# Performance work log

Measured on AMD Instinct MI355X. Metric: run time of the kernel, lower is better.

## Reference

```python
import jax, jax.numpy as jnp
import numpy as np

NODE_SIZE = 500000
LINK_SIZE = 500
DIM = 128
NORM_P = 1
MARGIN = 1.0
BATCH = 16384


def setup_inputs() -> dict:
    key = jax.random.key(0)
    k1, k2, k3, k4, k5, k6, k7, k8 = jax.random.split(key, 8)
    ur_e = 6.0 / np.sqrt(DIM)
    ur_m = 6.0 / DIM
    node_w = jax.random.uniform(k1, (NODE_SIZE, DIM), jnp.float32, -ur_e, ur_e)
    link_w = jax.random.uniform(k2, (LINK_SIZE, DIM), jnp.float32, -ur_e, ur_e)
    transfer_w = jax.random.uniform(k3, (LINK_SIZE, DIM * DIM), jnp.float32, -ur_m, ur_m)
    sp = jax.random.randint(k4, (BATCH,), 0, NODE_SIZE)
    tp = jax.random.randint(k5, (BATCH,), 0, NODE_SIZE)
    sn = jax.random.randint(k6, (BATCH,), 0, NODE_SIZE)
    tn = jax.random.randint(k7, (BATCH,), 0, NODE_SIZE)
    r = jax.random.randint(k8, (BATCH,), 0, LINK_SIZE)
    return {"node_w": node_w, "link_w": link_w, "transfer_w": transfer_w,
            "sp": sp, "tp": tp, "sn": sn, "tn": tn, "r": r}


def _distance(node_w, link_w, transfer_w, s, r, t):
    # gather embeddings
    s_emb = node_w[s]                      # [B, D]
    t_emb = node_w[t]                      # [B, D]
    r_emb = link_w[r]                      # [B, D]
    M = transfer_w[r].reshape(-1, DIM, DIM)  # [B, D, D]
    # per-sample (1xD)x(DxD) matvec: e @ M
    s_proj = jnp.einsum('bd,bde->be', s_emb, M)
    t_proj = jnp.einsum('bd,bde->be', t_emb, M)
    diff = s_proj + r_emb - t_proj
    if NORM_P == 1:
        return jnp.sum(jnp.abs(diff), axis=1)
    return jnp.sum(jnp.abs(diff) ** NORM_P, axis=1) ** (1.0 / NORM_P)


def reference(node_w, link_w, transfer_w, sp, tp, sn, tn, r):
    pos = _distance(node_w, link_w, transfer_w, sp, r, tp)
    neg = _distance(node_w, link_w, transfer_w, sn, r, tn)
    # MarginRankingLoss with target = -1: max(0, (pos - neg) + margin)
    loss = jnp.maximum(pos - neg + MARGIN, 0.0)
    return jnp.mean(loss)
```

## Files before the change

kernel.cpp:

```cpp
#include <hip/hip_runtime.h>

#define BATCH 16384
#define DIM 128
#define NLINK 500
#define NG 16
#define CAP 128

__device__ __forceinline__ void gload_lds16(const float* g, float* l) {
    __builtin_amdgcn_global_load_lds(
        (const __attribute__((address_space(1))) void*)g,
        (__attribute__((address_space(3))) void*)l, 16, 0, 0);
}

__global__ void k_init(float* __restrict__ out) {
    if (threadIdx.x == 0) out[0] = 0.0f;
}

#define FMA4(acc, m, s)                                          \
    acc.x = fmaf(m.x, s, acc.x); acc.y = fmaf(m.y, s, acc.y);    \
    acc.z = fmaf(m.z, s, acc.z); acc.w = fmaf(m.w, s, acc.w);

#define STEP(M_, C_)                                             \
    FMA4(a0, M_, v0.C_) FMA4(a1, M_, v1.C_)                      \
    FMA4(a2, M_, v2.C_) FMA4(a3, M_, v3.C_)                      \
    FMA4(a4, M_, v4.C_) FMA4(a5, M_, v5.C_)                      \
    FMA4(a6, M_, v6.C_) FMA4(a7, M_, v7.C_)

__global__ __launch_bounds__(512, 2) void k_fused(
    const float* __restrict__ node_w, const float* __restrict__ link_w,
    const float* __restrict__ transfer_w,
    const int* __restrict__ sp, const int* __restrict__ tp,
    const int* __restrict__ sn, const int* __restrict__ tn,
    const int* __restrict__ r, float* __restrict__ out)
{
    __shared__ float Ms[DIM * DIM];
    __shared__ float dv[NG * 8 * DIM];
    __shared__ int   slist[CAP];
    __shared__ int   cnt;
    __shared__ float lossbuf[NG];

    const int link = blockIdx.x;
    const int t = threadIdx.x;
    const int g = t >> 5;
    const int q = t & 31;

    if (t == 0) cnt = 0;
    __syncthreads();

    int4 rv[8];
    #pragma unroll
    for (int j = 0; j < 8; j++) rv[j] = ((const int4*)r)[j * 512 + t];

    {
        const float* src = transfer_w + (size_t)link * (DIM * DIM);
        #pragma unroll
        for (int i = 0; i < 8; i++) {
            const int c = (t + 512 * i) * 4;
            gload_lds16(src + c, Ms + c);
        }
    }

    #pragma unroll
    for (int j = 0; j < 8; j++) {
        const int bi = (j * 512 + t) * 4;
        if (rv[j].x == link) slist[atomicAdd(&cnt, 1)] = bi;
        if (rv[j].y == link) slist[atomicAdd(&cnt, 1)] = bi + 1;
        if (rv[j].z == link) slist[atomicAdd(&cnt, 1)] = bi + 2;
        if (rv[j].w == link) slist[atomicAdd(&cnt, 1)] = bi + 3;
    }
    __syncthreads();

    const int count = cnt;
    float* gbase = dv + (g * 8) * DIM;
    const float4* M4 = (const float4*)Ms;
    float lsum = 0.0f;

    for (int u0 = 4 * g; u0 < count; u0 += 4 * NG) {
        const float4 re = ((const float4*)(link_w + (size_t)link * DIM))[q];

        const int b0 = slist[u0];
        const int b1 = slist[(u0 + 1 < count) ? u0 + 1 : count - 1];
        const int b2 = slist[(u0 + 2 < count) ? u0 + 2 : count - 1];
        const int b3 = slist[(u0 + 3 < count) ? u0 + 3 : count - 1];

        #define ROW(idx) (((const float4*)(node_w + (size_t)(idx) * DIM))[q])
        float4 A0 = ROW(sp[b0]), C0 = ROW(tp[b0]), E0 = ROW(sn[b0]), F0 = ROW(tn[b0]);
        float4 A1 = ROW(sp[b1]), C1 = ROW(tp[b1]), E1 = ROW(sn[b1]), F1 = ROW(tn[b1]);
        float4 A2 = ROW(sp[b2]), C2 = ROW(tp[b2]), E2 = ROW(sn[b2]), F2 = ROW(tn[b2]);
        float4 A3 = ROW(sp[b3]), C3 = ROW(tp[b3]), E3 = ROW(sn[b3]), F3 = ROW(tn[b3]);
        #undef ROW

        {
            float4 w_;
            #define DIFF(vec, X, Y)                                              \
                w_.x = X.x - Y.x; w_.y = X.y - Y.y;                              \
                w_.z = X.z - Y.z; w_.w = X.w - Y.w;                              \
                ((float4*)(gbase + (vec) * DIM))[q] = w_;
            DIFF(0, A0, C0) DIFF(1, E0, F0)
            DIFF(2, A1, C1) DIFF(3, E1, F1)
            DIFF(4, A2, C2) DIFF(5, E2, F2)
            DIFF(6, A3, C3) DIFF(7, E3, F3)
            #undef DIFF
        }

        float4 a0 = {0,0,0,0}, a1 = {0,0,0,0}, a2 = {0,0,0,0}, a3 = {0,0,0,0};
        float4 a4 = {0,0,0,0}, a5 = {0,0,0,0}, a6 = {0,0,0,0}, a7 = {0,0,0,0};
        const float4* V0 = (const float4*)(gbase + 0 * DIM);
        const float4* V1 = (const float4*)(gbase + 1 * DIM);
        const float4* V2 = (const float4*)(gbase + 2 * DIM);
        const float4* V3 = (const float4*)(gbase + 3 * DIM);
        const float4* V4 = (const float4*)(gbase + 4 * DIM);
        const float4* V5 = (const float4*)(gbase + 5 * DIM);
        const float4* V6 = (const float4*)(gbase + 6 * DIM);
        const float4* V7 = (const float4*)(gbase + 7 * DIM);

        #pragma unroll 2
        for (int d4 = 0; d4 < 32; d4++) {
            float4 v0 = V0[d4], v1 = V1[d4], v2 = V2[d4], v3 = V3[d4];
            float4 v4 = V4[d4], v5 = V5[d4], v6 = V6[d4], v7 = V7[d4];
            float4 m0 = M4[(4 * d4 + 0) * 32 + q];
            float4 m1 = M4[(4 * d4 + 1) * 32 + q];
            float4 m2 = M4[(4 * d4 + 2) * 32 + q];
            float4 m3 = M4[(4 * d4 + 3) * 32 + q];
            STEP(m0, x) STEP(m1, y) STEP(m2, z) STEP(m3, w)
        }

        #define LOSS(ACp, ACn)                                                   \
            (fabsf(ACp.x + re.x) + fabsf(ACp.y + re.y) +                         \
             fabsf(ACp.z + re.z) + fabsf(ACp.w + re.w)                           \
           - fabsf(ACn.x + re.x) - fabsf(ACn.y + re.y)                           \
           - fabsf(ACn.z + re.z) - fabsf(ACn.w + re.w))
        float s0 = LOSS(a0, a1);
        float s1 = LOSS(a2, a3);
        float s2 = LOSS(a4, a5);
        float s3 = LOSS(a6, a7);
        #undef LOSS
        #pragma unroll
        for (int o = 16; o >= 1; o >>= 1) {
            s0 += __shfl_xor(s0, o, 32);
            s1 += __shfl_xor(s1, o, 32);
            s2 += __shfl_xor(s2, o, 32);
            s3 += __shfl_xor(s3, o, 32);
        }
        if (q == 0) {
            lsum += fmaxf(s0 + 1.0f, 0.0f);
            if (u0 + 1 < count) lsum += fmaxf(s1 + 1.0f, 0.0f);
            if (u0 + 2 < count) lsum += fmaxf(s2 + 1.0f, 0.0f);
            if (u0 + 3 < count) lsum += fmaxf(s3 + 1.0f, 0.0f);
        }
    }

    if (q == 0) lossbuf[g] = lsum;
    __syncthreads();
    if (t == 0) {
        float s = 0.0f;
        #pragma unroll
        for (int i = 0; i < NG; i++) s += lossbuf[i];
        atomicAdd(out, s * (1.0f / BATCH));
    }
}

extern "C" void kernel_launch(void* const* d_in, const int* in_sizes, int n_in,
                              void* d_out, int out_size, void* d_ws, size_t ws_size,
                              hipStream_t stream) {
    const float* node_w     = (const float*)d_in[0];
    const float* link_w     = (const float*)d_in[1];
    const float* transfer_w = (const float*)d_in[2];
    const int* sp = (const int*)d_in[3];
    const int* tp = (const int*)d_in[4];
    const int* sn = (const int*)d_in[5];
    const int* tn = (const int*)d_in[6];
    const int* r  = (const int*)d_in[7];
    float* out = (float*)d_out;
    (void)d_ws; (void)ws_size;

    k_init<<<1, 64, 0, stream>>>(out);
    k_fused<<<NLINK, 512, 0, stream>>>(node_w, link_w, transfer_w,
                                       sp, tp, sn, tn, r, out);
}
```

Baseline: 346.6 us.

## Pipeline transfer-matrix LDS loads with gathers and prefetch next rows

Each 32-lane group now handles two samples per pass instead of four. The node-row gathers are issued before the transfer-matrix global-to-LDS copy. The matvec is split into four chunks gated by vmcnt waits and barriers, so computation starts on parts of M while the rest is still loading. Node rows for the next iteration are prefetched into registers during the current sweep. The goal is to hide global-load latency and overlap the M copy with compute, at the cost of fragile hand-placed waitcnt and barrier scheduling and less work per group per pass.

```diff
diff --git a/kernel.cpp b/kernel.cpp
--- a/kernel.cpp
+++ b/kernel.cpp
@@ -12,6 +12,10 @@
         (__attribute__((address_space(3))) void*)l, 16, 0, 0);
 }
 
+#define SBAR()    __builtin_amdgcn_s_barrier()
+#define SCHEDB()  __builtin_amdgcn_sched_barrier(0)
+#define VMWAIT(n) asm volatile("s_waitcnt vmcnt(" #n ")" ::: "memory")
+
 __global__ void k_init(float* __restrict__ out) {
     if (threadIdx.x == 0) out[0] = 0.0f;
 }
@@ -20,11 +24,41 @@
     acc.x = fmaf(m.x, s, acc.x); acc.y = fmaf(m.y, s, acc.y);    \
     acc.z = fmaf(m.z, s, acc.z); acc.w = fmaf(m.w, s, acc.w);
 
-#define STEP(M_, C_)                                             \
-    FMA4(a0, M_, v0.C_) FMA4(a1, M_, v1.C_)                      \
-    FMA4(a2, M_, v2.C_) FMA4(a3, M_, v3.C_)                      \
-    FMA4(a4, M_, v4.C_) FMA4(a5, M_, v5.C_)                      \
-    FMA4(a6, M_, v6.C_) FMA4(a7, M_, v7.C_)
+template <int LO, int HI>
+__device__ __forceinline__ void sweep(const float4* M4, int q,
+    const float4* Vp0, const float4* Vn0, const float4* Vp1, const float4* Vn1,
+    float4& ap0, float4& an0, float4& ap1, float4& an1)
+{
+    #pragma unroll
+    for (int d4 = LO; d4 < HI; d4++) {
+        float4 vp0 = Vp0[d4], vn0 = Vn0[d4];
+        float4 vp1 = Vp1[d4], vn1 = Vn1[d4];
+        float4 m0 = M4[(4 * d4 + 0) * 32 + q];
+        float4 m1 = M4[(4 * d4 + 1) * 32 + q];
+        float4 m2 = M4[(4 * d4 + 2) * 32 + q];
+        float4 m3 = M4[(4 * d4 + 3) * 32 + q];
+        FMA4(ap0, m0, vp0.x) FMA4(an0, m0, vn0.x)
+        FMA4(ap1, m0, vp1.x) FMA4(an1, m0, vn1.x)
+        FMA4(ap0, m1, vp0.y) FMA4(an0, m1, vn0.y)
+        FMA4(ap1, m1, vp1.y) FMA4(an1, m1, vn1.y)
+        FMA4(ap0, m2, vp0.z) FMA4(an0, m2, vn0.z)
+        FMA4(ap1, m2, vp1.z) FMA4(an1, m2, vn1.z)
+        FMA4(ap0, m3, vp0.w) FMA4(an0, m3, vn0.w)
+        FMA4(ap1, m3, vp1.w) FMA4(an1, m3, vn1.w)
+    }
+}
+
+#define ROW(idx) (((const float4*)(node_w + (size_t)(idx) * DIM))[q])
+#define DIFFW(dst, X, Y) {                                       \
+    float4 w_;                                                   \
+    w_.x = X.x - Y.x; w_.y = X.y - Y.y;                          \
+    w_.z = X.z - Y.z; w_.w = X.w - Y.w;                          \
+    ((float4*)(dst))[q] = w_; }
+#define LOSS(ACp, ACn)                                           \
+    (fabsf(ACp.x + re.x) + fabsf(ACp.y + re.y) +                 \
+     fabsf(ACp.z + re.z) + fabsf(ACp.w + re.w)                   \
+   - fabsf(ACn.x + re.x) - fabsf(ACn.y + re.y)                   \
+   - fabsf(ACn.z + re.z) - fabsf(ACn.w + re.w))
 
 __global__ __launch_bounds__(512, 2) void k_fused(
     const float* __restrict__ node_w, const float* __restrict__ link_w,
@@ -34,7 +68,7 @@
     const int* __restrict__ r, float* __restrict__ out)
 {
     __shared__ float Ms[DIM * DIM];
-    __shared__ float dv[NG * 8 * DIM];
+    __shared__ float dv[NG * 4 * DIM];
     __shared__ int   slist[CAP];
     __shared__ int   cnt;
     __shared__ float lossbuf[NG];
@@ -50,16 +84,6 @@
     int4 rv[8];
     #pragma unroll
     for (int j = 0; j < 8; j++) rv[j] = ((const int4*)r)[j * 512 + t];
-
-    {
-        const float* src = transfer_w + (size_t)link * (DIM * DIM);
-        #pragma unroll
-        for (int i = 0; i < 8; i++) {
-            const int c = (t + 512 * i) * 4;
-            gload_lds16(src + c, Ms + c);
-        }
-    }
-
     #pragma unroll
     for (int j = 0; j < 8; j++) {
         const int bi = (j * 512 + t) * 4;
@@ -69,85 +93,111 @@
         if (rv[j].w == link) slist[atomicAdd(&cnt, 1)] = bi + 3;
     }
     __syncthreads();
-
     const int count = cnt;
-    float* gbase = dv + (g * 8) * DIM;
-    const float4* M4 = (const float4*)Ms;
+
+    const bool act0 = (g < count);
+    const bool act1 = (g + 16 < count);
+    int b0 = 0, b1 = 0, nb0 = 0, nb1 = 0;
+    if (count > 0) {
+        b0  = slist[act0 ? g : 0];
+        b1  = act1 ? slist[g + 16] : b0;
+        const int nk = g + 32;
+        nb0 = (nk < count) ? slist[nk] : b0;
+        nb1 = (nk + 16 < count) ? slist[nk + 16] : nb0;
+    }
+    int isp0 = sp[b0], itp0 = tp[b0], isn0 = sn[b0], itn0 = tn[b0];
+    int isp1 = sp[b1], itp1 = tp[b1], isn1 = sn[b1], itn1 = tn[b1];
+    SCHEDB();
+    float4 A0 = ROW(isp0), C0 = ROW(itp0), E0 = ROW(isn0), F0 = ROW(itn0);
+    float4 A1 = ROW(isp1), C1 = ROW(itp1), E1 = ROW(isn1), F1 = ROW(itn1);
+    SCHEDB();
+    int jsp0 = sp[nb0], jtp0 = tp[nb0], jsn0 = sn[nb0], jtn0 = tn[nb0];
+    int jsp1 = sp[nb1], jtp1 = tp[nb1], jsn1 = sn[nb1], jtn1 = tn[nb1];
+    const float4 re = ((const float4*)(link_w + (size_t)link * DIM))[q];
+    SCHEDB();
+    {
+        const float* src = transfer_w + (size_t)link * (DIM * DIM);
+        #pragma unroll
+        for (int i = 0; i < 8; i++) {
+            const int c = (t + 512 * i) * 4;
+            gload_lds16(src + c, Ms + c);
+            SCHEDB();
+        }
+    }
+
+    float* p0r = dv + (g * 4 + 0) * DIM;
+    float* n0r = dv + (g * 4 + 1) * DIM;
+    float* p1r = dv + (g * 4 + 2) * DIM;
+    float* n1r = dv + (g * 4 + 3) * DIM;
+    DIFFW(p0r, A0, C0) DIFFW(n0r, E0, F0)
+    DIFFW(p1r, A1, C1) DIFFW(n1r, E1, F1)
+
+    const float4* M4  = (const float4*)Ms;
+    const float4* Vp0 = (const float4*)p0r;
+    const float4* Vn0 = (const float4*)n0r;
+    const float4* Vp1 = (const float4*)p1r;
+    const float4* Vn1 = (const float4*)n1r;
+    float4 ap0 = {0,0,0,0}, an0 = {0,0,0,0}, ap1 = {0,0,0,0}, an1 = {0,0,0,0};
+
+    VMWAIT(6); SCHEDB(); SBAR();
+    sweep<0, 8>(M4, q, Vp0, Vn0, Vp1, Vn1, ap0, an0, ap1, an1);
+    VMWAIT(4); SCHEDB(); SBAR();
+    sweep<8, 16>(M4, q, Vp0, Vn0, Vp1, Vn1, ap0, an0, ap1, an1);
+    VMWAIT(2); SCHEDB(); SBAR();
+    sweep<16, 24>(M4, q, Vp0, Vn0, Vp1, Vn1, ap0, an0, ap1, an1);
+    float4 pa0 = ROW(jsp0), pc0 = ROW(jtp0), pe0 = ROW(jsn0), pf0 = ROW(jtn0);
+    float4 pa1 = ROW(jsp1), pc1 = ROW(jtp1), pe1 = ROW(jsn1), pf1 = ROW(jtn1);
+    SCHEDB();
+    VMWAIT(8); SCHEDB(); SBAR();
+    sweep<24, 32>(M4, q, Vp0, Vn0, Vp1, Vn1, ap0, an0, ap1, an1);
+
     float lsum = 0.0f;
-
-    for (int u0 = 4 * g; u0 < count; u0 += 4 * NG) {
-        const float4 re = ((const float4*)(link_w + (size_t)link * DIM))[q];
-
-        const int b0 = slist[u0];
-        const int b1 = slist[(u0 + 1 < count) ? u0 + 1 : count - 1];
-        const int b2 = slist[(u0 + 2 < count) ? u0 + 2 : count - 1];
-        const int b3 = slist[(u0 + 3 < count) ? u0 + 3 : count - 1];
-
-        #define ROW(idx) (((const float4*)(node_w + (size_t)(idx) * DIM))[q])
-        float4 A0 = ROW(sp[b0]), C0 = ROW(tp[b0]), E0 = ROW(sn[b0]), F0 = ROW(tn[b0]);
-        float4 A1 = ROW(sp[b1]), C1 = ROW(tp[b1]), E1 = ROW(sn[b1]), F1 = ROW(tn[b1]);
-        float4 A2 = ROW(sp[b2]), C2 = ROW(tp[b2]), E2 = ROW(sn[b2]), F2 = ROW(tn[b2]);
-        float4 A3 = ROW(sp[b3]), C3 = ROW(tp[b3]), E3 = ROW(sn[b3]), F3 = ROW(tn[b3]);
-        #undef ROW
-
+    {
+        float v0 = LOSS(ap0, an0);
+        float v1 = LOSS(ap1, an1);
+        #pragma unroll
+        for (int o = 16; o >= 1; o >>= 1) {
+            v0 += __shfl_xor(v0, o, 32);
+            v1 += __shfl_xor(v1, o, 32);
+        }
+        if (q == 0) {
+            if (act0) lsum += fmaxf(v0 + 1.0f, 0.0f);
+            if (act1) lsum += fmaxf(v1 + 1.0f, 0.0f);
+        }
+    }
+
+    int myk = g + 32;
+    while (myk < count) {
+        const bool a1 = (myk + 16) < count;
+        DIFFW(p0r, pa0, pc0) DIFFW(n0r, pe0, pf0)
+        DIFFW(p1r, pa1, pc1) DIFFW(n1r, pe1, pf1)
+        const int nx = myk + 32;
+        const bool h2 = nx < count;
         {
-            float4 w_;
-            #define DIFF(vec, X, Y)                                              \
-                w_.x = X.x - Y.x; w_.y = X.y - Y.y;                              \
-                w_.z = X.z - Y.z; w_.w = X.w - Y.w;                              \
-                ((float4*)(gbase + (vec) * DIM))[q] = w_;
-            DIFF(0, A0, C0) DIFF(1, E0, F0)
-            DIFF(2, A1, C1) DIFF(3, E1, F1)
-            DIFF(4, A2, C2) DIFF(5, E2, F2)
-            DIFF(6, A3, C3) DIFF(7, E3, F3)
-            #undef DIFF
-        }
-
-        float4 a0 = {0,0,0,0}, a1 = {0,0,0,0}, a2 = {0,0,0,0}, a3 = {0,0,0,0};
-        float4 a4 = {0,0,0,0}, a5 = {0,0,0,0}, a6 = {0,0,0,0}, a7 = {0,0,0,0};
-        const float4* V0 = (const float4*)(gbase + 0 * DIM);
-        const float4* V1 = (const float4*)(gbase + 1 * DIM);
-        const float4* V2 = (const float4*)(gbase + 2 * DIM);
-        const float4* V3 = (const float4*)(gbase + 3 * DIM);
-        const float4* V4 = (const float4*)(gbase + 4 * DIM);
-        const float4* V5 = (const float4*)(gbase + 5 * DIM);
-        const float4* V6 = (const float4*)(gbase + 6 * DIM);
-        const float4* V7 = (const float4*)(gbase + 7 * DIM);
-
-        #pragma unroll 2
-        for (int d4 = 0; d4 < 32; d4++) {
-            float4 v0 = V0[d4], v1 = V1[d4], v2 = V2[d4], v3 = V3[d4];
-            float4 v4 = V4[d4], v5 = V5[d4], v6 = V6[d4], v7 = V7[d4];
-            float4 m0 = M4[(4 * d4 + 0) * 32 + q];
-            float4 m1 = M4[(4 * d4 + 1) * 32 + q];
-            float4 m2 = M4[(4 * d4 + 2) * 32 + q];
-            float4 m3 = M4[(4 * d4 + 3) * 32 + q];
-            STEP(m0, x) STEP(m1, y) STEP(m2, z) STEP(m3, w)
-        }
-
-        #define LOSS(ACp, ACn)                                                   \
-            (fabsf(ACp.x + re.x) + fabsf(ACp.y + re.y) +                         \
-             fabsf(ACp.z + re.z) + fabsf(ACp.w + re.w)                           \
-           - fabsf(ACn.x + re.x) - fabsf(ACn.y + re.y)                           \
-           - fabsf(ACn.z + re.z) - fabsf(ACn.w + re.w))
-        float s0 = LOSS(a0, a1);
-        float s1 = LOSS(a2, a3);
-        float s2 = LOSS(a4, a5);
-        float s3 = LOSS(a6, a7);
-        #undef LOSS
+            const int mb0 = h2 ? slist[nx] : 0;
+            const int mb1 = (h2 && nx + 16 < count) ? slist[nx + 16] : mb0;
+            if (h2) {
+                const int ksp0 = sp[mb0], ktp0 = tp[mb0], ksn0 = sn[mb0], ktn0 = tn[mb0];
+                const int ksp1 = sp[mb1], ktp1 = tp[mb1], ksn1 = sn[mb1], ktn1 = tn[mb1];
+                pa0 = ROW(ksp0); pc0 = ROW(ktp0); pe0 = ROW(ksn0); pf0 = ROW(ktn0);
+                pa1 = ROW(ksp1); pc1 = ROW(ktp1); pe1 = ROW(ksn1); pf1 = ROW(ktn1);
+            }
+        }
+        ap0 = {0,0,0,0}; an0 = {0,0,0,0}; ap1 = {0,0,0,0}; an1 = {0,0,0,0};
+        sweep<0, 32>(M4, q, Vp0, Vn0, Vp1, Vn1, ap0, an0, ap1, an1);
+
+        float v0 = LOSS(ap0, an0);
+        float v1 = LOSS(ap1, an1);
         #pragma unroll
         for (int o = 16; o >= 1; o >>= 1) {
-            s0 += __shfl_xor(s0, o, 32);
-            s1 += __shfl_xor(s1, o, 32);
-            s2 += __shfl_xor(s2, o, 32);
-            s3 += __shfl_xor(s3, o, 32);
+            v0 += __shfl_xor(v0, o, 32);
+            v1 += __shfl_xor(v1, o, 32);
         }
         if (q == 0) {
-            lsum += fmaxf(s0 + 1.0f, 0.0f);
-            if (u0 + 1 < count) lsum += fmaxf(s1 + 1.0f, 0.0f);
-            if (u0 + 2 < count) lsum += fmaxf(s2 + 1.0f, 0.0f);
-            if (u0 + 3 < count) lsum += fmaxf(s3 + 1.0f, 0.0f);
-        }
+            lsum += fmaxf(v0 + 1.0f, 0.0f);
+            if (a1) lsum += fmaxf(v1 + 1.0f, 0.0f);
+        }
+        myk = nx;
     }
 
     if (q == 0) lossbuf[g] = lsum;
```

New measurement: 351.8 us. No clear change (+1.5%).
